# Optimization experiments

Hardware: AMD Instinct MI355X
Metric: run time of the kernel (lower is better)

Reference implementation:

```python
import jax, jax.numpy as jnp
import numpy as np

B, D, R = 256, 4096, 8
MAX_R = 2 * R - 1  # static upper bound on radius (torch uses data-dependent max)


def setup_inputs() -> dict:
    key = jax.random.key(0)
    ks = jax.random.split(key, 6)
    x = jax.random.randint(ks[0], (B, D), 0, 2).astype(jnp.float32)  # binary spins
    W = jax.random.normal(ks[1], (D, D), jnp.float32) / np.float32(np.sqrt(D))
    b = jax.random.normal(ks[2], (D,), jnp.float32)
    radius_raw = jax.random.randint(ks[3], (B, 1), 0, MAX_R)  # +1 in reference -> [1, 2R-1]
    gumbel_u = jax.random.uniform(ks[4], (B, D), jnp.float32)
    u = jax.random.uniform(ks[5], (B,), jnp.float32)
    return {"x": x, "W": W, "b": b, "radius_raw": radius_raw, "gumbel_u": gumbel_u, "u": u}


def _model(x, W, b):
    # quadratic pseudo-Boolean energy model: per-sample scalar score
    return 0.5 * jnp.einsum('bi,ij,bj->b', x, W, x) + x @ b


def reference(x, W, b, radius_raw, gumbel_u, u):
    radius = radius_raw + 1                                   # [B,1] in [1, 2R-1]
    r_mask = (jnp.arange(MAX_R)[None, :] < radius).astype(x.dtype)  # [B, MAX_R]

    score_x = _model(x, W, b)                                 # [B]
    grad = jax.lax.stop_gradient(
        jax.grad(lambda xx: _model(xx, W, b).sum())(x))       # [B,D], detached

    delta_x = -(2.0 * x - 1.0)
    score_change_x = delta_x * grad / 2.0                     # logits of proposal

    # multinomial without replacement == Gumbel top-k on the logits
    eps = 1e-10
    g = -jnp.log(-jnp.log(jnp.clip(gumbel_u, eps, 1.0 - eps)))
    _, indices = jax.lax.top_k(score_change_x + g, MAX_R)     # [B, MAX_R]

    rows = jnp.arange(B)[:, None]
    cur_bits = x[rows, indices]                               # gather
    new_bits = 1.0 - cur_bits
    y = x.at[rows, indices].set(r_mask * new_bits + (1.0 - r_mask) * cur_bits)

    delta_y = -(2.0 * y - 1.0)
    score_y = _model(y, W, b)
    score_change_y = delta_y * grad / 2.0

    log_pypx = score_y - score_x
    log_tilde_pxpy = -jnp.sum(grad * (y - x), axis=-1)
    log_zxzy = (jax.scipy.special.logsumexp(score_change_x, axis=-1)
                - jax.scipy.special.logsumexp(score_change_y, axis=-1))
    log_acc = jnp.minimum(log_pypx + log_tilde_pxpy + log_zxzy, 0.0)

    accepted = (jnp.exp(log_acc) > u).astype(x.dtype)[:, None]  # [B,1]
    return y * accepted + (1.0 - accepted) * x
```

## Files before the change

### kernel.cpp

```cpp
#include <hip/hip_runtime.h>

#define Bsz 256
#define Dd  4096
#define MAXR 15
#define FMAX 3.402823466e+38f
#define KSPLIT 2
#define KCHUNK (Dd / KSPLIT)
#define BK 64
#define LSTRIDE 72

typedef short bf16x8 __attribute__((ext_vector_type(8)));
typedef float f32x4  __attribute__((ext_vector_type(4)));

__device__ __forceinline__ unsigned short f2bf(float f) {
    unsigned int u = __float_as_uint(f);
    unsigned int r = (u + 0x7fffu + ((u >> 16) & 1u)) >> 16;
    return (unsigned short)r;
}
__device__ __forceinline__ float bf2f(unsigned short h) {
    return __uint_as_float(((unsigned int)h) << 16);
}

__global__ __launch_bounds__(256) void k_ssym(const float* __restrict__ W,
                                              const float* __restrict__ x,
                                              unsigned short* __restrict__ shi,
                                              unsigned short* __restrict__ slo,
                                              unsigned short* __restrict__ xb) {
    __shared__ float t1[64][68];
    __shared__ float t2[64][68];
    int bid = blockIdx.x;
    int bi = 0;
    while (bid >= 64 - bi) { bid -= 64 - bi; ++bi; }
    const int bj = bi + bid;
    const int i0 = bi * 64, j0 = bj * 64;
    const int tid = threadIdx.x;

    #pragma unroll
    for (int sb = 0; sb < 4; ++sb) {
        int s = sb * 256 + tid;
        int r = s >> 4, q = (s & 15) * 4;
        *(float4*)&t1[r][q] = *(const float4*)(W + (size_t)(i0 + r) * Dd + j0 + q);
        *(float4*)&t2[r][q] = *(const float4*)(W + (size_t)(j0 + r) * Dd + i0 + q);
    }
    __syncthreads();

    const int r = tid >> 2, c0 = (tid & 3) * 16;
    {
        unsigned short vh[16], vl[16];
        #pragma unroll
        for (int k = 0; k < 16; ++k) {
            float s = 0.5f * (t1[r][c0 + k] + t2[c0 + k][r]);
            vh[k] = f2bf(s);
            vl[k] = f2bf(s - bf2f(vh[k]));
        }
        size_t o = (size_t)(i0 + r) * Dd + j0 + c0;
        *(uint4*)(shi + o) = *(const uint4*)&vh[0];
        *(uint4*)(shi + o + 8) = *(const uint4*)&vh[8];
        *(uint4*)(slo + o) = *(const uint4*)&vl[0];
        *(uint4*)(slo + o + 8) = *(const uint4*)&vl[8];
    }
    if (bi != bj) {
        unsigned short vh[16], vl[16];
        #pragma unroll
        for (int k = 0; k < 16; ++k) {
            float s = 0.5f * (t2[r][c0 + k] + t1[c0 + k][r]);
            vh[k] = f2bf(s);
            vl[k] = f2bf(s - bf2f(vh[k]));
        }
        size_t o = (size_t)(j0 + r) * Dd + i0 + c0;
        *(uint4*)(shi + o) = *(const uint4*)&vh[0];
        *(uint4*)(shi + o + 8) = *(const uint4*)&vh[8];
        *(uint4*)(slo + o) = *(const uint4*)&vl[0];
        *(uint4*)(slo + o + 8) = *(const uint4*)&vl[8];
    }

    if (blockIdx.x < 256) {
        const float* xp = x + (size_t)blockIdx.x * 4096;
        unsigned short* xo = xb + (size_t)blockIdx.x * 4096;
        #pragma unroll
        for (int c = 0; c < 4; ++c) {
            int e = c * 1024 + tid * 4;
            float4 v = *(const float4*)(xp + e);
            unsigned short o4[4] = { f2bf(v.x), f2bf(v.y), f2bf(v.z), f2bf(v.w) };
            *(uint2*)(xo + e) = *(const uint2*)o4;
        }
    }
}

__global__ __launch_bounds__(128) void k_gemm(const unsigned short* __restrict__ xb,
                                              const unsigned short* __restrict__ shi,
                                              const unsigned short* __restrict__ slo,
                                              float* __restrict__ part) {
    __shared__ __align__(16) unsigned short As[64 * LSTRIDE];
    __shared__ __align__(16) unsigned short Bh[64 * LSTRIDE];
    __shared__ __align__(16) unsigned short Bl[64 * LSTRIDE];
    const int tid = threadIdx.x;
    const int n0 = blockIdx.x * 64, m0 = blockIdx.y * 64;
    const int kbase = blockIdx.z * KCHUNK;
    const int w = tid >> 6, lane = tid & 63;
    const int ln = lane & 15, quad = lane >> 4;

    size_t ga[4], gb[4];
    int lofs[4];
    #pragma unroll
    for (int j = 0; j < 4; ++j) {
        int s = tid + j * 128;
        int r = s >> 3, g = s & 7;
        ga[j]   = (size_t)(m0 + r) * Dd + kbase + g * 8;
        gb[j]   = (size_t)(n0 + r) * Dd + kbase + g * 8;
        lofs[j] = r * LSTRIDE + g * 8;
    }

    f32x4 acc[4][2];
    #pragma unroll
    for (int mt = 0; mt < 4; ++mt)
        #pragma unroll
        for (int ct = 0; ct < 2; ++ct)
            #pragma unroll
            for (int rr = 0; rr < 4; ++rr) acc[mt][ct][rr] = 0.0f;

    for (int k0 = 0; k0 < KCHUNK; k0 += BK) {
        __syncthreads();
        bf16x8 va[4], vh[4], vl[4];
        #pragma unroll
        for (int j = 0; j < 4; ++j) {
            va[j] = *(const bf16x8*)(xb  + ga[j] + k0);
            vh[j] = *(const bf16x8*)(shi + gb[j] + k0);
            vl[j] = *(const bf16x8*)(slo + gb[j] + k0);
        }
        #pragma unroll
        for (int j = 0; j < 4; ++j) {
            *(bf16x8*)&As[lofs[j]] = va[j];
            *(bf16x8*)&Bh[lofs[j]] = vh[j];
            *(bf16x8*)&Bl[lofs[j]] = vl[j];
        }
        __syncthreads();
        #pragma unroll
        for (int kk = 0; kk < BK; kk += 32) {
            const int gr = (kk >> 3) + quad;
            bf16x8 a[4];
            #pragma unroll
            for (int mt = 0; mt < 4; ++mt)
                a[mt] = *(const bf16x8*)&As[(mt * 16 + ln) * LSTRIDE + gr * 8];
            #pragma unroll
            for (int ct = 0; ct < 2; ++ct) {
                int rb = w * 32 + ct * 16 + ln;
                bf16x8 bh = *(const bf16x8*)&Bh[rb * LSTRIDE + gr * 8];
                bf16x8 bl = *(const bf16x8*)&Bl[rb * LSTRIDE + gr * 8];
                #pragma unroll
                for (int mt = 0; mt < 4; ++mt) {
                    acc[mt][ct] = __builtin_amdgcn_mfma_f32_16x16x32_bf16(a[mt], bh, acc[mt][ct], 0, 0, 0);
                    acc[mt][ct] = __builtin_amdgcn_mfma_f32_16x16x32_bf16(a[mt], bl, acc[mt][ct], 0, 0, 0);
                }
            }
        }
    }
    float* prow = part + (size_t)blockIdx.z * (Bsz * Dd);
    #pragma unroll
    for (int mt = 0; mt < 4; ++mt)
        #pragma unroll
        for (int ct = 0; ct < 2; ++ct)
            #pragma unroll
            for (int rr = 0; rr < 4; ++rr) {
                int m = m0 + mt * 16 + quad * 4 + rr;
                int n = n0 + w * 32 + ct * 16 + ln;
                prow[(size_t)m * Dd + n] = acc[mt][ct][rr];
            }
}

__device__ __forceinline__ float block_max256(float v, float* redf) {
    #pragma unroll
    for (int off = 32; off; off >>= 1) v = fmaxf(v, __shfl_down(v, off));
    __syncthreads();
    if ((threadIdx.x & 63) == 0) redf[threadIdx.x >> 6] = v;
    __syncthreads();
    return fmaxf(fmaxf(redf[0], redf[1]), fmaxf(redf[2], redf[3]));
}
__device__ __forceinline__ float block_sum256(float v, float* redf) {
    #pragma unroll
    for (int off = 32; off; off >>= 1) v += __shfl_down(v, off);
    __syncthreads();
    if ((threadIdx.x & 63) == 0) redf[threadIdx.x >> 6] = v;
    __syncthreads();
    return (redf[0] + redf[1]) + (redf[2] + redf[3]);
}
__device__ __forceinline__ void block_argmax256(float v, int idx, float* redf, int* redi,
                                                float& bv, int& bi) {
    #pragma unroll
    for (int off = 32; off; off >>= 1) {
        float v2 = __shfl_down(v, off);
        int   i2 = __shfl_down(idx, off);
        if (v2 > v || (v2 == v && i2 < idx)) { v = v2; idx = i2; }
    }
    __syncthreads();
    if ((threadIdx.x & 63) == 0) { redf[threadIdx.x >> 6] = v; redi[threadIdx.x >> 6] = idx; }
    __syncthreads();
    bv = redf[0]; bi = redi[0];
    #pragma unroll
    for (int w2 = 1; w2 < 4; ++w2) {
        float v2 = redf[w2]; int i2 = redi[w2];
        if (v2 > bv || (v2 == bv && i2 < bi)) { bv = v2; bi = i2; }
    }
}

__global__ __launch_bounds__(256) void k_epilogue(const float* __restrict__ x,
                                                  const float* __restrict__ W,
                                                  const int* __restrict__ radius_raw,
                                                  const float* __restrict__ gu,
                                                  const float* __restrict__ uvec,
                                                  const float* __restrict__ part,
                                                  const float* __restrict__ bias,
                                                  float* __restrict__ out) {
    __shared__ float scx_s[Dd];
    __shared__ float key_s[Dd];
    __shared__ float redf[4];
    __shared__ int   redi[4];
    __shared__ int   flips[MAXR];

    const int b = blockIdx.x;
    const int tid = threadIdx.x;
    const float* xrow  = x  + (size_t)b * Dd;
    const float* gurow = gu + (size_t)b * Dd;
    const float* p0 = part + (size_t)b * Dd;
    const float* p1 = part + (size_t)(Bsz + b) * Dd;

    float lmax = -FMAX;
    #pragma unroll
    for (int c = 0; c < 4; ++c) {
        int j = c * 1024 + tid * 4;
        float4 a0 = *(const float4*)(p0 + j);
        float4 a1 = *(const float4*)(p1 + j);
        float4 bs = *(const float4*)(bias + j);
        float4 xv = *(const float4*)(xrow + j);
        float4 uu = *(const float4*)(gurow + j);
        float g0 = a0.x + a1.x + bs.x, g1 = a0.y + a1.y + bs.y;
        float g2 = a0.z + a1.z + bs.z, g3 = a0.w + a1.w + bs.w;
        float4 sc, ky;
        sc.x = (1.0f - 2.0f * xv.x) * g0 * 0.5f;
        sc.y = (1.0f - 2.0f * xv.y) * g1 * 0.5f;
        sc.z = (1.0f - 2.0f * xv.z) * g2 * 0.5f;
        sc.w = (1.0f - 2.0f * xv.w) * g3 * 0.5f;
        ky.x = sc.x - logf(-logf(fmaxf(uu.x, 1e-10f)));
        ky.y = sc.y - logf(-logf(fmaxf(uu.y, 1e-10f)));
        ky.z = sc.z - logf(-logf(fmaxf(uu.z, 1e-10f)));
        ky.w = sc.w - logf(-logf(fmaxf(uu.w, 1e-10f)));
        *(float4*)&scx_s[j] = sc;
        *(float4*)&key_s[j] = ky;
        lmax = fmaxf(lmax, fmaxf(fmaxf(sc.x, sc.y), fmaxf(sc.z, sc.w)));
    }
    float mx = block_max256(lmax, redf);
    float ls = 0.0f;
    for (int j = tid; j < Dd; j += 256) ls += expf(scx_s[j] - mx);
    float lse_x = mx + logf(block_sum256(ls, redf));

    const int radius = radius_raw[b] + 1;
    for (int t = 0; t < radius; ++t) {
        float v = -FMAX; int idx = 0x7fffffff;
        for (int j = tid; j < Dd; j += 256) {
            float kv = key_s[j];
            if (kv > v) { v = kv; idx = j; }
        }
        float bv; int bi;
        block_argmax256(v, idx, redf, redi, bv, bi);
        if (tid == 0) { flips[t] = bi; key_s[bi] = -FMAX; }
        __syncthreads();
    }

    float lmy = -FMAX;
    for (int j = tid; j < Dd; j += 256) {
        float v = scx_s[j];
        for (int t = 0; t < radius; ++t) if (j == flips[t]) v = -v;
        lmy = fmaxf(lmy, v);
    }
    float my = block_max256(lmy, redf);
    float lsy = 0.0f;
    for (int j = tid; j < Dd; j += 256) {
        float v = scx_s[j];
        for (int t = 0; t < radius; ++t) if (j == flips[t]) v = -v;
        lsy += expf(v - my);
    }
    float lse_y = my + logf(block_sum256(lsy, redf));

    float ts = 0.0f;
    for (int t = tid; t < radius * radius; t += 256) {
        int p = flips[t / radius], q = flips[t % radius];
        float dp = 1.0f - 2.0f * xrow[p];
        float dq = 1.0f - 2.0f * xrow[q];
        ts += 0.25f * dp * dq * (W[(size_t)p * Dd + q] + W[(size_t)q * Dd + p]);
    }
    float T = block_sum256(ts, redf);

    float log_acc = fminf(T + lse_x - lse_y, 0.0f);
    int accepted = (expf(log_acc) > uvec[b]) ? 1 : 0;

    __syncthreads();
    float* orow = out + (size_t)b * Dd;
    #pragma unroll
    for (int c = 0; c < 4; ++c) {
        int j = c * 1024 + tid * 4;
        *(float4*)(orow + j) = *(const float4*)(xrow + j);
    }
    __syncthreads();
    if (accepted && tid < radius) {
        int p = flips[tid];
        orow[p] = 1.0f - xrow[p];
    }
}

extern "C" void kernel_launch(void* const* d_in, const int* in_sizes, int n_in,
                              void* d_out, int out_size, void* d_ws, size_t ws_size,
                              hipStream_t stream) {
    const float* x          = (const float*)d_in[0];
    const float* W          = (const float*)d_in[1];
    const float* bias       = (const float*)d_in[2];
    const int*   radius_raw = (const int*)d_in[3];
    const float* gu         = (const float*)d_in[4];
    const float* u          = (const float*)d_in[5];
    float* out = (float*)d_out;

    unsigned short* shi = (unsigned short*)d_ws;
    unsigned short* slo = shi + (size_t)Dd * Dd;
    unsigned short* xb  = slo + (size_t)Dd * Dd;
    float*          prt = (float*)(xb + (size_t)Bsz * Dd);

    k_ssym<<<2080, 256, 0, stream>>>(W, x, shi, slo, xb);
    k_gemm<<<dim3(64, 4, KSPLIT), 128, 0, stream>>>(xb, shi, slo, prt);
    k_epilogue<<<Bsz, 256, 0, stream>>>(x, W, radius_raw, gu, u, prt, bias, out);
}
```

Baseline: 203.1 us.

## Keep Gumbel keys in registers and compute logsumexp of y incrementally

The epilogue keeps its per-thread slice of the Gumbel keys in registers instead of shared memory. Each top-k round does a single block argmax reduction using a per-thread cached best value, and only the winning thread rescans its 16 keys. The second logsumexp is now an incremental correction of the first sum over the flipped indices, which removes two full passes over D that had a nested loop over the flips. The output copy reuses the x values already loaded and drops a barrier. Register use goes up, and reusing mx as the shift for the y sum could lose precision if flipped logits become large.

```diff
diff --git a/kernel.cpp b/kernel.cpp
--- a/kernel.cpp
+++ b/kernel.cpp
@@ -184,24 +184,6 @@
     __syncthreads();
     return (redf[0] + redf[1]) + (redf[2] + redf[3]);
 }
-__device__ __forceinline__ void block_argmax256(float v, int idx, float* redf, int* redi,
-                                                float& bv, int& bi) {
-    #pragma unroll
-    for (int off = 32; off; off >>= 1) {
-        float v2 = __shfl_down(v, off);
-        int   i2 = __shfl_down(idx, off);
-        if (v2 > v || (v2 == v && i2 < idx)) { v = v2; idx = i2; }
-    }
-    __syncthreads();
-    if ((threadIdx.x & 63) == 0) { redf[threadIdx.x >> 6] = v; redi[threadIdx.x >> 6] = idx; }
-    __syncthreads();
-    bv = redf[0]; bi = redi[0];
-    #pragma unroll
-    for (int w2 = 1; w2 < 4; ++w2) {
-        float v2 = redf[w2]; int i2 = redi[w2];
-        if (v2 > bv || (v2 == bv && i2 < bi)) { bv = v2; bi = i2; }
-    }
-}
 
 __global__ __launch_bounds__(256) void k_epilogue(const float* __restrict__ x,
                                                   const float* __restrict__ W,
@@ -212,9 +194,9 @@
                                                   const float* __restrict__ bias,
                                                   float* __restrict__ out) {
     __shared__ float scx_s[Dd];
-    __shared__ float key_s[Dd];
-    __shared__ float redf[4];
-    __shared__ int   redi[4];
+    __shared__ float redf[2][4];
+    __shared__ int   redi[2][4];
+    __shared__ float redsum[4];
     __shared__ int   flips[MAXR];
 
     const int b = blockIdx.x;
@@ -224,62 +206,90 @@
     const float* p0 = part + (size_t)b * Dd;
     const float* p1 = part + (size_t)(Bsz + b) * Dd;
 
-    float lmax = -FMAX;
+    float4 a0[4], a1[4], bs4[4], xv4[4], uu4[4];
     #pragma unroll
     for (int c = 0; c < 4; ++c) {
         int j = c * 1024 + tid * 4;
-        float4 a0 = *(const float4*)(p0 + j);
-        float4 a1 = *(const float4*)(p1 + j);
-        float4 bs = *(const float4*)(bias + j);
-        float4 xv = *(const float4*)(xrow + j);
-        float4 uu = *(const float4*)(gurow + j);
-        float g0 = a0.x + a1.x + bs.x, g1 = a0.y + a1.y + bs.y;
-        float g2 = a0.z + a1.z + bs.z, g3 = a0.w + a1.w + bs.w;
-        float4 sc, ky;
-        sc.x = (1.0f - 2.0f * xv.x) * g0 * 0.5f;
-        sc.y = (1.0f - 2.0f * xv.y) * g1 * 0.5f;
-        sc.z = (1.0f - 2.0f * xv.z) * g2 * 0.5f;
-        sc.w = (1.0f - 2.0f * xv.w) * g3 * 0.5f;
-        ky.x = sc.x - logf(-logf(fmaxf(uu.x, 1e-10f)));
-        ky.y = sc.y - logf(-logf(fmaxf(uu.y, 1e-10f)));
-        ky.z = sc.z - logf(-logf(fmaxf(uu.z, 1e-10f)));
-        ky.w = sc.w - logf(-logf(fmaxf(uu.w, 1e-10f)));
-        *(float4*)&scx_s[j] = sc;
-        *(float4*)&key_s[j] = ky;
-        lmax = fmaxf(lmax, fmaxf(fmaxf(sc.x, sc.y), fmaxf(sc.z, sc.w)));
-    }
-    float mx = block_max256(lmax, redf);
+        a0[c]  = *(const float4*)(p0 + j);
+        a1[c]  = *(const float4*)(p1 + j);
+        bs4[c] = *(const float4*)(bias + j);
+        xv4[c] = *(const float4*)(xrow + j);
+        uu4[c] = *(const float4*)(gurow + j);
+    }
+    float sc[16], ky[16];
+    float lmax = -FMAX;
+    float lkey = -FMAX; int lidx = 0x7fffffff;
+    #pragma unroll
+    for (int c = 0; c < 4; ++c) {
+        const float* ga = (const float*)&a0[c];
+        const float* gb = (const float*)&a1[c];
+        const float* gc = (const float*)&bs4[c];
+        const float* gx = (const float*)&xv4[c];
+        const float* gup = (const float*)&uu4[c];
+        #pragma unroll
+        for (int e = 0; e < 4; ++e) {
+            int r = c * 4 + e;
+            float g = ga[e] + gb[e] + gc[e];
+            float s = (1.0f - 2.0f * gx[e]) * g * 0.5f;
+            float k = s - logf(-logf(fmaxf(gup[e], 1e-10f)));
+            sc[r] = s;
+            ky[r] = k;
+            lmax = fmaxf(lmax, s);
+            if (k > lkey) { lkey = k; lidx = c * 1024 + tid * 4 + e; }
+        }
+        *(float4*)&scx_s[c * 1024 + tid * 4] = *(const float4*)&sc[c * 4];
+    }
+
+    float mx = block_max256(lmax, redsum);
     float ls = 0.0f;
-    for (int j = tid; j < Dd; j += 256) ls += expf(scx_s[j] - mx);
-    float lse_x = mx + logf(block_sum256(ls, redf));
+    #pragma unroll
+    for (int r = 0; r < 16; ++r) ls += expf(sc[r] - mx);
+    float sum_x = block_sum256(ls, redsum);
+    float lse_x = mx + logf(sum_x);
 
     const int radius = radius_raw[b] + 1;
+    unsigned removed = 0;
     for (int t = 0; t < radius; ++t) {
-        float v = -FMAX; int idx = 0x7fffffff;
-        for (int j = tid; j < Dd; j += 256) {
-            float kv = key_s[j];
-            if (kv > v) { v = kv; idx = j; }
-        }
-        float bv; int bi;
-        block_argmax256(v, idx, redf, redi, bv, bi);
-        if (tid == 0) { flips[t] = bi; key_s[bi] = -FMAX; }
+        float v = lkey; int idx = lidx;
+        #pragma unroll
+        for (int off = 32; off; off >>= 1) {
+            float v2 = __shfl_down(v, off);
+            int   i2 = __shfl_down(idx, off);
+            if (v2 > v || (v2 == v && i2 < idx)) { v = v2; idx = i2; }
+        }
+        const int buf = t & 1;
+        if ((tid & 63) == 0) { redf[buf][tid >> 6] = v; redi[buf][tid >> 6] = idx; }
         __syncthreads();
-    }
-
-    float lmy = -FMAX;
-    for (int j = tid; j < Dd; j += 256) {
-        float v = scx_s[j];
-        for (int t = 0; t < radius; ++t) if (j == flips[t]) v = -v;
-        lmy = fmaxf(lmy, v);
-    }
-    float my = block_max256(lmy, redf);
-    float lsy = 0.0f;
-    for (int j = tid; j < Dd; j += 256) {
-        float v = scx_s[j];
-        for (int t = 0; t < radius; ++t) if (j == flips[t]) v = -v;
-        lsy += expf(v - my);
-    }
-    float lse_y = my + logf(block_sum256(lsy, redf));
+        float bv = redf[buf][0]; int bi = redi[buf][0];
+        #pragma unroll
+        for (int w2 = 1; w2 < 4; ++w2) {
+            float v2 = redf[buf][w2]; int i2 = redi[buf][w2];
+            if (v2 > bv || (v2 == bv && i2 < bi)) { bv = v2; bi = i2; }
+        }
+        if (tid == ((bi >> 2) & 255)) {
+            removed |= 1u << (((bi >> 10) << 2) | (bi & 3));
+            lkey = -FMAX; lidx = 0x7fffffff;
+            #pragma unroll
+            for (int c = 0; c < 4; ++c)
+                #pragma unroll
+                for (int e = 0; e < 4; ++e) {
+                    int r = c * 4 + e;
+                    if (!(removed & (1u << r)) && ky[r] > lkey) {
+                        lkey = ky[r]; lidx = c * 1024 + tid * 4 + e;
+                    }
+                }
+        }
+        if (tid == 0) flips[t] = bi;
+    }
+    __syncthreads();
+
+    float delta = 0.0f;
+    if (tid < radius) {
+        float sv = scx_s[flips[tid]];
+        delta = expf(-sv - mx) - expf(sv - mx);
+    }
+    float sum_y = sum_x + block_sum256(delta, redsum);
+    float lse_y = mx + logf(sum_y);
 
     float ts = 0.0f;
     for (int t = tid; t < radius * radius; t += 256) {
@@ -288,18 +298,15 @@
         float dq = 1.0f - 2.0f * xrow[q];
         ts += 0.25f * dp * dq * (W[(size_t)p * Dd + q] + W[(size_t)q * Dd + p]);
     }
-    float T = block_sum256(ts, redf);
+    float T = block_sum256(ts, redsum);
 
     float log_acc = fminf(T + lse_x - lse_y, 0.0f);
     int accepted = (expf(log_acc) > uvec[b]) ? 1 : 0;
 
-    __syncthreads();
     float* orow = out + (size_t)b * Dd;
     #pragma unroll
-    for (int c = 0; c < 4; ++c) {
-        int j = c * 1024 + tid * 4;
-        *(float4*)(orow + j) = *(const float4*)(xrow + j);
-    }
+    for (int c = 0; c < 4; ++c)
+        *(float4*)(orow + c * 1024 + tid * 4) = xv4[c];
     __syncthreads();
     if (accepted && tid < radius) {
         int p = flips[tid];
```

Result: faster. 180.9 us (-10.9%).
